# Performance work log

Measured on AMD Instinct MI355X. Metric: run time of the kernel, lower is better.

## Reference

```python
import jax, jax.numpy as jnp
import numpy as np

N, E, F, H, C = 100000, 1600000, 128, 128, 40


def setup_inputs() -> dict:
    key = jax.random.key(0)
    ks = jax.random.split(key, 9)
    feat = jax.random.normal(ks[0], (N, F), dtype=jnp.float32)
    src = jax.random.randint(ks[1], (E,), 0, N, dtype=jnp.int32)
    dst = jax.random.randint(ks[2], (E,), 0, N, dtype=jnp.int32)
    def glorot(k, fan_in, fan_out):
        s = np.float32(np.sqrt(6.0 / (fan_in + fan_out)))
        return jax.random.uniform(k, (fan_in, fan_out), jnp.float32, -s, s)
    W0 = glorot(ks[3], F, H); b0 = jnp.zeros((H,), jnp.float32)
    W1 = glorot(ks[4], H, H); b1 = jnp.zeros((H,), jnp.float32)
    W2 = glorot(ks[5], H, C); b2 = jnp.zeros((C,), jnp.float32)
    return {"feat": feat, "src": src, "dst": dst,
            "W0": W0, "b0": b0, "W1": W1, "b1": b1, "W2": W2, "b2": b2}


def _graph_conv(h, src, dst, norm_out, norm_in, W, b):
    # DGL GraphConv, norm='both': out = D_in^{-1/2} A D_out^{-1/2} h W + b
    h = h * norm_out[:, None]          # scale by source out-degree
    h = h @ W                          # transform first (in_dim >= out_dim path)
    agg = jax.ops.segment_sum(h[src], dst, num_segments=N)  # scatter-add over edges
    return agg * norm_in[:, None] + b


def reference(feat, src, dst, W0, b0, W1, b1, W2, b2):
    ones_e = jnp.ones((E,), jnp.float32)
    deg_out = jax.ops.segment_sum(ones_e, src, num_segments=N)
    deg_in = jax.ops.segment_sum(ones_e, dst, num_segments=N)
    norm_out = jnp.where(deg_out > 0, jax.lax.rsqrt(jnp.maximum(deg_out, 1.0)), 0.0)
    norm_in = jnp.where(deg_in > 0, jax.lax.rsqrt(jnp.maximum(deg_in, 1.0)), 0.0)
    h = _graph_conv(feat, src, dst, norm_out, norm_in, W0, b0)
    h = jax.nn.relu(h)
    h = _graph_conv(h, src, dst, norm_out, norm_in, W1, b1)
    h = jax.nn.relu(h)
    h = _graph_conv(h, src, dst, norm_out, norm_in, W2, b2)
    return h
```

## Files before the change

kernel.cpp:

```cpp
#include <hip/hip_runtime.h>


#define KDIM 128
#define EPB 4096

__device__ __forceinline__ float bf2f(unsigned short u) {
    unsigned int x = ((unsigned int)u) << 16;
    return __builtin_bit_cast(float, x);
}
__device__ __forceinline__ unsigned short f2bf(float f) {
    unsigned int x = __builtin_bit_cast(unsigned int, f);
    unsigned int r = x + 0x7FFFu + ((x >> 16) & 1u);
    return (unsigned short)(r >> 16);
}

__global__ __launch_bounds__(256) void b0_count(const int* __restrict__ src,
                                                const int* __restrict__ dst,
                                                int* __restrict__ gcntA,
                                                int* __restrict__ gcntB, int E, int nb) {
    __shared__ int hA[512], hB[512];
    const int t = threadIdx.x;
    for (int b = t; b < nb; b += 256) { hA[b] = 0; hB[b] = 0; }
    __syncthreads();
    const int base = blockIdx.x * EPB;
#pragma unroll
    for (int i = 0; i < 16; ++i) {
        int e = base + i * 256 + t;
        if (e < E) {
            atomicAdd(&hA[dst[e] >> 8], 1);
            atomicAdd(&hB[src[e] >> 8], 1);
        }
    }
    __syncthreads();
    for (int b = t; b < nb; b += 256) {
        if (hA[b]) atomicAdd(&gcntA[b], hA[b]);
        if (hB[b]) atomicAdd(&gcntB[b], hB[b]);
    }
}

__global__ __launch_bounds__(512) void b0b_offsets(const int* __restrict__ gcntA,
                                                   const int* __restrict__ gcntB,
                                                   int* __restrict__ offA,
                                                   int* __restrict__ offB,
                                                   int* __restrict__ gcurA,
                                                   int* __restrict__ gcurB,
                                                   int* __restrict__ row_off,
                                                   int nb, int N, int E) {
    __shared__ int sm[512];
    const int t = threadIdx.x;
    int v = (t < nb) ? gcntA[t] : 0;
    sm[t] = v;
    __syncthreads();
    for (int o = 1; o < 512; o <<= 1) {
        int x = (t >= o) ? sm[t - o] : 0;
        __syncthreads();
        sm[t] += x;
        __syncthreads();
    }
    if (t < nb) { offA[t + 1] = sm[t]; gcurA[t] = sm[t] - v; }
    if (t == 0) { offA[0] = 0; row_off[N] = E; }
    __syncthreads();
    int vb = (t < nb) ? gcntB[t] : 0;
    sm[t] = vb;
    __syncthreads();
    for (int o = 1; o < 512; o <<= 1) {
        int x = (t >= o) ? sm[t - o] : 0;
        __syncthreads();
        sm[t] += x;
        __syncthreads();
    }
    if (t < nb) { offB[t + 1] = sm[t]; gcurB[t] = sm[t] - vb; }
    if (t == 0) offB[0] = 0;
}

__global__ __launch_bounds__(256) void b1_bin(const int* __restrict__ src,
                                              const int* __restrict__ dst,
                                              int* __restrict__ gcurA,
                                              int* __restrict__ gcurB,
                                              int* __restrict__ binA,
                                              int* __restrict__ binB, int E, int nb) {
    __shared__ int hA[512], hB[512];
    const int t = threadIdx.x;
    for (int b = t; b < nb; b += 256) { hA[b] = 0; hB[b] = 0; }
    __syncthreads();
    const int base = blockIdx.x * EPB;
    int se[16], de[16];
#pragma unroll
    for (int i = 0; i < 16; ++i) {
        int e = base + i * 256 + t;
        se[i] = -1; de[i] = 0;
        if (e < E) {
            se[i] = src[e]; de[i] = dst[e];
            atomicAdd(&hA[de[i] >> 8], 1);
            atomicAdd(&hB[se[i] >> 8], 1);
        }
    }
    __syncthreads();
    for (int b = t; b < nb; b += 256) {
        int c = hA[b];
        hA[b] = c ? atomicAdd(&gcurA[b], c) : 0;
        c = hB[b];
        hB[b] = c ? atomicAdd(&gcurB[b], c) : 0;
    }
    __syncthreads();
#pragma unroll
    for (int i = 0; i < 16; ++i) {
        if (se[i] >= 0) {
            int pA = atomicAdd(&hA[de[i] >> 8], 1);
            binA[pA] = se[i] | ((de[i] & 255) << 17);
            int pB = atomicAdd(&hB[se[i] >> 8], 1);
            binB[pB] = se[i] & 255;
        }
    }
}

__global__ __launch_bounds__(256) void b2_final(const int* __restrict__ binA,
                                                const int* __restrict__ binB,
                                                const int* __restrict__ offA,
                                                const int* __restrict__ offB,
                                                int* __restrict__ ssrc,
                                                int* __restrict__ row_off,
                                                float* __restrict__ norm_in,
                                                int* __restrict__ degO, int N) {
    __shared__ int h[256], cur[256];
    const int b = blockIdx.x, t = threadIdx.x;
    const int nA0 = offA[b], cntA = offA[b + 1] - nA0;
    const int nodes = min(256, N - b * 256);

    h[t] = 0;
    __syncthreads();
    for (int k = t; k < cntA; k += 256) atomicAdd(&h[binA[nA0 + k] >> 17], 1);
    __syncthreads();

    int v = h[t];
    cur[t] = v;
    __syncthreads();
    for (int o = 1; o < 256; o <<= 1) {
        int x = (t >= o) ? cur[t - o] : 0;
        __syncthreads();
        cur[t] += x;
        __syncthreads();
    }
    const int rbase = nA0 + (cur[t] - v);
    if (t < nodes) {
        row_off[b * 256 + t] = rbase;
        norm_in[b * 256 + t] = (v > 0) ? rsqrtf((float)v) : 0.0f;
    }
    __syncthreads();
    cur[t] = rbase;
    __syncthreads();

    for (int k = t; k < cntA; k += 256) {
        int val = binA[nA0 + k];
        int pos = atomicAdd(&cur[val >> 17], 1);
        ssrc[pos] = val & 0x1FFFF;
    }

    __syncthreads();
    h[t] = 0;
    __syncthreads();
    const int nB0 = offB[b], cntB = offB[b + 1] - nB0;
    for (int k = t; k < cntB; k += 256) atomicAdd(&h[binB[nB0 + k]], 1);
    __syncthreads();
    if (t < nodes) degO[b * 256 + t] = h[t];
}

template <int M, int RPB, int CPT, bool BF16OUT>
__global__ __launch_bounds__(256) void gemm_scaled(const float* __restrict__ X,
                                                   const int* __restrict__ degO,
                                                   const float* __restrict__ W,
                                                   void* __restrict__ Tout, int nrows) {
    constexpr int CG = M / CPT;
    static_assert(CG * (RPB / 2) == 256, "thread mapping");
    __shared__ float xs[KDIM][RPB + 1];
    __shared__ float ws[64][M];

    const int t = threadIdx.x;
    const int rowbase = blockIdx.x * RPB;

    {
        constexpr int NV = RPB * (KDIM / 4) / 256;
        const float4* X4 = reinterpret_cast<const float4*>(X);
#pragma unroll
        for (int i = 0; i < NV; ++i) {
            int idx = t + i * 256;
            int rl = idx >> 5;
            int kq = idx & 31;
            int row = rowbase + rl;
            float4 v = make_float4(0.f, 0.f, 0.f, 0.f);
            float s = 0.f;
            if (row < nrows) {
                v = X4[(size_t)row * 32 + kq];
                int dv = degO[row];
                s = (dv > 0) ? rsqrtf((float)dv) : 0.0f;
            }
            xs[4 * kq + 0][rl] = v.x * s;
            xs[4 * kq + 1][rl] = v.y * s;
            xs[4 * kq + 2][rl] = v.z * s;
            xs[4 * kq + 3][rl] = v.w * s;
        }
    }

    const int rg = t / CG, cg = t % CG;
    const int r0 = 2 * rg, cb = cg * CPT;
    float acc0[CPT] = {0.f}, acc1[CPT] = {0.f};

    for (int kc = 0; kc < 2; ++kc) {
        __syncthreads();
        {
            constexpr int TOT4 = 64 * M / 4;
            const float4* W4 = reinterpret_cast<const float4*>(W);
            for (int i = t; i < TOT4; i += 256) {
                int kk = i / (M / 4), m4 = i % (M / 4);
                float4 v = W4[(size_t)(kc * 64 + kk) * (M / 4) + m4];
                ws[kk][4 * m4 + 0] = v.x;
                ws[kk][4 * m4 + 1] = v.y;
                ws[kk][4 * m4 + 2] = v.z;
                ws[kk][4 * m4 + 3] = v.w;
            }
        }
        __syncthreads();
#pragma unroll 8
        for (int k = 0; k < 64; ++k) {
            float xv0 = xs[kc * 64 + k][r0];
            float xv1 = xs[kc * 64 + k][r0 + 1];
#pragma unroll
            for (int j = 0; j < CPT; ++j) {
                float wv = ws[k][cb + j];
                acc0[j] = fmaf(xv0, wv, acc0[j]);
                acc1[j] = fmaf(xv1, wv, acc1[j]);
            }
        }
    }

    int row0 = rowbase + r0;
    if constexpr (BF16OUT) {
        static_assert(CPT == 8, "bf16 path packs 8");
        unsigned short* Tb = (unsigned short*)Tout;
        if (row0 < nrows) {
            uint4 pk;
            pk.x = f2bf(acc0[0]) | ((unsigned)f2bf(acc0[1]) << 16);
            pk.y = f2bf(acc0[2]) | ((unsigned)f2bf(acc0[3]) << 16);
            pk.z = f2bf(acc0[4]) | ((unsigned)f2bf(acc0[5]) << 16);
            pk.w = f2bf(acc0[6]) | ((unsigned)f2bf(acc0[7]) << 16);
            *reinterpret_cast<uint4*>(&Tb[(size_t)row0 * M + cb]) = pk;
        }
        if (row0 + 1 < nrows) {
            uint4 pk;
            pk.x = f2bf(acc1[0]) | ((unsigned)f2bf(acc1[1]) << 16);
            pk.y = f2bf(acc1[2]) | ((unsigned)f2bf(acc1[3]) << 16);
            pk.z = f2bf(acc1[4]) | ((unsigned)f2bf(acc1[5]) << 16);
            pk.w = f2bf(acc1[6]) | ((unsigned)f2bf(acc1[7]) << 16);
            *reinterpret_cast<uint4*>(&Tb[(size_t)(row0 + 1) * M + cb]) = pk;
        }
    } else {
        float* T = (float*)Tout;
        if (row0 < nrows) {
#pragma unroll
            for (int j = 0; j < CPT; ++j) T[(size_t)row0 * M + cb + j] = acc0[j];
        }
        if (row0 + 1 < nrows) {
#pragma unroll
            for (int j = 0; j < CPT; ++j) T[(size_t)(row0 + 1) * M + cb + j] = acc1[j];
        }
    }
}

__global__ __launch_bounds__(256) void agg_bf16(const unsigned short* __restrict__ Tb,
                                                const int* __restrict__ row_off,
                                                const int* __restrict__ ssrc,
                                                const float* __restrict__ norm_in,
                                                const float* __restrict__ bias,
                                                float* __restrict__ out, int n) {
    const int wid = (int)((blockIdx.x * blockDim.x + threadIdx.x) >> 6);
    const int lane = threadIdx.x & 63;
    if (wid >= n) return;
    const uint* T2 = reinterpret_cast<const uint*>(Tb);
    const int e0 = row_off[wid], e1 = row_off[wid + 1];
    float ax = 0.f, ay = 0.f;
    int e = e0;
    for (; e + 4 <= e1; e += 4) {
        int s0 = ssrc[e], s1 = ssrc[e + 1], s2 = ssrc[e + 2], s3 = ssrc[e + 3];
        uint v0 = T2[(size_t)s0 * 64 + lane];
        uint v1 = T2[(size_t)s1 * 64 + lane];
        uint v2 = T2[(size_t)s2 * 64 + lane];
        uint v3 = T2[(size_t)s3 * 64 + lane];
        ax += bf2f((unsigned short)v0) + bf2f((unsigned short)v1)
            + bf2f((unsigned short)v2) + bf2f((unsigned short)v3);
        ay += bf2f((unsigned short)(v0 >> 16)) + bf2f((unsigned short)(v1 >> 16))
            + bf2f((unsigned short)(v2 >> 16)) + bf2f((unsigned short)(v3 >> 16));
    }
    for (; e < e1; ++e) {
        uint v = T2[(size_t)ssrc[e] * 64 + lane];
        ax += bf2f((unsigned short)v);
        ay += bf2f((unsigned short)(v >> 16));
    }
    float ni = norm_in[wid];
    float2 b = reinterpret_cast<const float2*>(bias)[lane];
    float ox = fmaxf(ax * ni + b.x, 0.f);
    float oy = fmaxf(ay * ni + b.y, 0.f);
    reinterpret_cast<float2*>(out)[(size_t)wid * 64 + lane] = make_float2(ox, oy);
}

template <int M, bool RELU>
__global__ __launch_bounds__(256) void agg_kernel(const float* __restrict__ T,
                                                  const int* __restrict__ row_off,
                                                  const int* __restrict__ ssrc,
                                                  const float* __restrict__ norm_in,
                                                  const float* __restrict__ bias,
                                                  float* __restrict__ out, int n) {
    const int wid = (int)((blockIdx.x * blockDim.x + threadIdx.x) >> 6);
    const int lane = threadIdx.x & 63;
    if (wid >= n) return;
    constexpr int L = M / 2;
    const float2* T2 = reinterpret_cast<const float2*>(T);
    const int e0 = row_off[wid], e1 = row_off[wid + 1];
    if (lane < L) {
        float ax = 0.f, ay = 0.f;
        int e = e0;
        for (; e + 4 <= e1; e += 4) {
            int s0 = ssrc[e], s1 = ssrc[e + 1], s2 = ssrc[e + 2], s3 = ssrc[e + 3];
            float2 v0 = T2[s0 * L + lane];
            float2 v1 = T2[s1 * L + lane];
            float2 v2 = T2[s2 * L + lane];
            float2 v3 = T2[s3 * L + lane];
            ax += (v0.x + v1.x) + (v2.x + v3.x);
            ay += (v0.y + v1.y) + (v2.y + v3.y);
        }
        for (; e < e1; ++e) {
            int s = ssrc[e];
            float2 v = T2[s * L + lane];
            ax += v.x;
            ay += v.y;
        }
        float ni = norm_in[wid];
        float2 b = reinterpret_cast<const float2*>(bias)[lane];
        float ox = ax * ni + b.x;
        float oy = ay * ni + b.y;
        if (RELU) { ox = fmaxf(ox, 0.f); oy = fmaxf(oy, 0.f); }
        reinterpret_cast<float2*>(out)[(size_t)wid * L + lane] = make_float2(ox, oy);
    }
}

extern "C" void kernel_launch(void* const* d_in, const int* in_sizes, int n_in,
                              void* d_out, int out_size, void* d_ws, size_t ws_size,
                              hipStream_t stream) {
    const float* feat = (const float*)d_in[0];
    const int* src = (const int*)d_in[1];
    const int* dst = (const int*)d_in[2];
    const float* W0 = (const float*)d_in[3];
    const float* b0 = (const float*)d_in[4];
    const float* W1 = (const float*)d_in[5];
    const float* b1 = (const float*)d_in[6];
    const float* W2 = (const float*)d_in[7];
    const float* b2 = (const float*)d_in[8];
    float* outp = (float*)d_out;

    const int N = in_sizes[0] / KDIM;
    const int E = in_sizes[1];
    const int nb = (N + 255) >> 8;
    const int nblkE = (E + EPB - 1) / EPB;

    auto align = [](size_t x) { return (x + 255) & ~(size_t)255; };
    char* p = (char*)d_ws;
    int* degO      = (int*)p;    p += align((size_t)N * 4);
    float* norm_in = (float*)p;  p += align((size_t)N * 4);
    int* row_off   = (int*)p;    p += align((size_t)(N + 1) * 4);
    int* gcntA     = (int*)p;    p += 512 * 4;
    int* gcntB     = (int*)p;    p += 512 * 4;
    int* offA      = (int*)p;    p += align(513 * 4);
    int* offB      = (int*)p;    p += align(513 * 4);
    int* gcurA     = (int*)p;    p += align(512 * 4);
    int* gcurB     = (int*)p;    p += align(512 * 4);
    int* ssrc      = (int*)p;    p += align((size_t)E * 4);
    float* T       = (float*)p;  p += align((size_t)N * KDIM * 4);
    float* H       = (float*)p;  p += align((size_t)N * KDIM * 4);
    unsigned short* Tb = (unsigned short*)T;
    int* binA      = (int*)T;
    int* binB      = binA + E;
    (void)n_in; (void)out_size; (void)ws_size;

    const int aggBlocks = (int)(((size_t)N * 64 + 255) / 256);

    hipMemsetAsync(gcntA, 0, 1024 * 4, stream);

    b0_count<<<nblkE, 256, 0, stream>>>(src, dst, gcntA, gcntB, E, nb);
    b0b_offsets<<<1, 512, 0, stream>>>(gcntA, gcntB, offA, offB, gcurA, gcurB, row_off, nb, N, E);
    b1_bin<<<nblkE, 256, 0, stream>>>(src, dst, gcurA, gcurB, binA, binB, E, nb);
    b2_final<<<nb, 256, 0, stream>>>(binA, binB, offA, offB, ssrc, row_off, norm_in, degO, N);

    gemm_scaled<128, 32, 8, true><<<(N + 31) / 32, 256, 0, stream>>>(feat, degO, W0, Tb, N);
    agg_bf16<<<aggBlocks, 256, 0, stream>>>(Tb, row_off, ssrc, norm_in, b0, H, N);

    gemm_scaled<128, 32, 8, true><<<(N + 31) / 32, 256, 0, stream>>>(H, degO, W1, Tb, N);
    agg_bf16<<<aggBlocks, 256, 0, stream>>>(Tb, row_off, ssrc, norm_in, b1, H, N);

    gemm_scaled<40, 64, 5, false><<<(N + 63) / 64, 256, 0, stream>>>(H, degO, W2, T, N);
    agg_kernel<40, false><<<aggBlocks, 256, 0, stream>>>(T, row_off, ssrc, norm_in, b2, outp, N);
}
```

Measured before the change: 591.2 us.

## Use bf16 MFMA for the two 128x128 GraphConv transforms

```diff
diff --git a/kernel.cpp b/kernel.cpp
--- a/kernel.cpp
+++ b/kernel.cpp
@@ -3,6 +3,9 @@
 
 #define KDIM 128
 #define EPB 4096
+
+typedef __attribute__((ext_vector_type(4))) float f32x4;
+typedef __attribute__((ext_vector_type(8))) short short8;
 
 __device__ __forceinline__ float bf2f(unsigned short u) {
     unsigned int x = ((unsigned int)u) << 16;
@@ -165,103 +168,71 @@
     if (t < nodes) degO[b * 256 + t] = h[t];
 }
 
-template <int M, int RPB, int CPT, bool BF16OUT>
-__global__ __launch_bounds__(256) void gemm_scaled(const float* __restrict__ X,
-                                                   const int* __restrict__ degO,
-                                                   const float* __restrict__ W,
-                                                   void* __restrict__ Tout, int nrows) {
-    constexpr int CG = M / CPT;
-    static_assert(CG * (RPB / 2) == 256, "thread mapping");
-    __shared__ float xs[KDIM][RPB + 1];
-    __shared__ float ws[64][M];
-
+__global__ __launch_bounds__(256) void prep_w(const float* __restrict__ W,
+                                              unsigned int* __restrict__ Wtg) {
+    int idx = blockIdx.x * 256 + threadIdx.x;
+    if (idx < 8192) {
+        int c = idx >> 6, kk = idx & 63;
+        unsigned short lo = f2bf(W[(2 * kk) * 128 + c]);
+        unsigned short hi = f2bf(W[(2 * kk + 1) * 128 + c]);
+        Wtg[idx] = (unsigned)lo | ((unsigned)hi << 16);
+    }
+}
+
+__global__ __launch_bounds__(256, 4) void gemm_mfma(const float* __restrict__ X,
+                                                    const int* __restrict__ degO,
+                                                    const unsigned int* __restrict__ Wtg,
+                                                    unsigned short* __restrict__ Tb,
+                                                    int ntiles, int gridWaves) {
+    __shared__ unsigned int Wt[128 * 68];
     const int t = threadIdx.x;
-    const int rowbase = blockIdx.x * RPB;
-
-    {
-        constexpr int NV = RPB * (KDIM / 4) / 256;
-        const float4* X4 = reinterpret_cast<const float4*>(X);
-#pragma unroll
-        for (int i = 0; i < NV; ++i) {
-            int idx = t + i * 256;
-            int rl = idx >> 5;
-            int kq = idx & 31;
-            int row = rowbase + rl;
-            float4 v = make_float4(0.f, 0.f, 0.f, 0.f);
-            float s = 0.f;
-            if (row < nrows) {
-                v = X4[(size_t)row * 32 + kq];
-                int dv = degO[row];
-                s = (dv > 0) ? rsqrtf((float)dv) : 0.0f;
+    for (int idx = t; idx < 128 * 64; idx += 256) {
+        int c = idx >> 6, kk = idx & 63;
+        Wt[c * 68 + kk] = Wtg[idx];
+    }
+    __syncthreads();
+
+    const int lane = t & 63;
+    const int w = t >> 6;
+    const int l15 = lane & 15;
+    const int lh = lane >> 4;
+    const unsigned short* Wts = reinterpret_cast<const unsigned short*>(Wt);
+    const float4* X4 = reinterpret_cast<const float4*>(X);
+
+    for (int tile = blockIdx.x * 4 + w; tile < ntiles; tile += gridWaves) {
+        const int row = tile * 16 + l15;
+        const int dv = degO[row];
+        const float s = (dv > 0) ? rsqrtf((float)dv) : 0.0f;
+        const float4* Xr = X4 + ((size_t)row * 32 + lh * 2);
+
+        f32x4 acc[8];
+#pragma unroll
+        for (int ct = 0; ct < 8; ++ct) acc[ct] = f32x4{0.f, 0.f, 0.f, 0.f};
+
+#pragma unroll
+        for (int kc = 0; kc < 4; ++kc) {
+            float4 a0 = Xr[kc * 8];
+            float4 a1 = Xr[kc * 8 + 1];
+            short8 af;
+            af[0] = (short)f2bf(a0.x * s); af[1] = (short)f2bf(a0.y * s);
+            af[2] = (short)f2bf(a0.z * s); af[3] = (short)f2bf(a0.w * s);
+            af[4] = (short)f2bf(a1.x * s); af[5] = (short)f2bf(a1.y * s);
+            af[6] = (short)f2bf(a1.z * s); af[7] = (short)f2bf(a1.w * s);
+            const int k0 = kc * 32 + lh * 8;
+#pragma unroll
+            for (int ct = 0; ct < 8; ++ct) {
+                short8 bf = *reinterpret_cast<const short8*>(&Wts[(ct * 16 + l15) * 136 + k0]);
+                acc[ct] = __builtin_amdgcn_mfma_f32_16x16x32_bf16(af, bf, acc[ct], 0, 0, 0);
             }
-            xs[4 * kq + 0][rl] = v.x * s;
-            xs[4 * kq + 1][rl] = v.y * s;
-            xs[4 * kq + 2][rl] = v.z * s;
-            xs[4 * kq + 3][rl] = v.w * s;
-        }
-    }
-
-    const int rg = t / CG, cg = t % CG;
-    const int r0 = 2 * rg, cb = cg * CPT;
-    float acc0[CPT] = {0.f}, acc1[CPT] = {0.f};
-
-    for (int kc = 0; kc < 2; ++kc) {
-        __syncthreads();
-        {
-            constexpr int TOT4 = 64 * M / 4;
-            const float4* W4 = reinterpret_cast<const float4*>(W);
-            for (int i = t; i < TOT4; i += 256) {
-                int kk = i / (M / 4), m4 = i % (M / 4);
-                float4 v = W4[(size_t)(kc * 64 + kk) * (M / 4) + m4];
-                ws[kk][4 * m4 + 0] = v.x;
-                ws[kk][4 * m4 + 1] = v.y;
-                ws[kk][4 * m4 + 2] = v.z;
-                ws[kk][4 * m4 + 3] = v.w;
-            }
-        }
-        __syncthreads();
-#pragma unroll 8
-        for (int k = 0; k < 64; ++k) {
-            float xv0 = xs[kc * 64 + k][r0];
-            float xv1 = xs[kc * 64 + k][r0 + 1];
-#pragma unroll
-            for (int j = 0; j < CPT; ++j) {
-                float wv = ws[k][cb + j];
-                acc0[j] = fmaf(xv0, wv, acc0[j]);
-                acc1[j] = fmaf(xv1, wv, acc1[j]);
-            }
-        }
-    }
-
-    int row0 = rowbase + r0;
-    if constexpr (BF16OUT) {
-        static_assert(CPT == 8, "bf16 path packs 8");
-        unsigned short* Tb = (unsigned short*)Tout;
-        if (row0 < nrows) {
-            uint4 pk;
-            pk.x = f2bf(acc0[0]) | ((unsigned)f2bf(acc0[1]) << 16);
-            pk.y = f2bf(acc0[2]) | ((unsigned)f2bf(acc0[3]) << 16);
-            pk.z = f2bf(acc0[4]) | ((unsigned)f2bf(acc0[5]) << 16);
-            pk.w = f2bf(acc0[6]) | ((unsigned)f2bf(acc0[7]) << 16);
-            *reinterpret_cast<uint4*>(&Tb[(size_t)row0 * M + cb]) = pk;
-        }
-        if (row0 + 1 < nrows) {
-            uint4 pk;
-            pk.x = f2bf(acc1[0]) | ((unsigned)f2bf(acc1[1]) << 16);
-            pk.y = f2bf(acc1[2]) | ((unsigned)f2bf(acc1[3]) << 16);
-            pk.z = f2bf(acc1[4]) | ((unsigned)f2bf(acc1[5]) << 16);
-            pk.w = f2bf(acc1[6]) | ((unsigned)f2bf(acc1[7]) << 16);
-            *reinterpret_cast<uint4*>(&Tb[(size_t)(row0 + 1) * M + cb]) = pk;
-        }
-    } else {
-        float* T = (float*)Tout;
-        if (row0 < nrows) {
-#pragma unroll
-            for (int j = 0; j < CPT; ++j) T[(size_t)row0 * M + cb + j] = acc0[j];
-        }
-        if (row0 + 1 < nrows) {
-#pragma unroll
-            for (int j = 0; j < CPT; ++j) T[(size_t)(row0 + 1) * M + cb + j] = acc1[j];
+        }
+
+        const int rbase = tile * 16 + lh * 4;
+#pragma unroll
+        for (int ct = 0; ct < 8; ++ct) {
+            const int col = ct * 16 + l15;
+#pragma unroll
+            for (int r = 0; r < 4; ++r)
+                Tb[(size_t)(rbase + r) * 128 + col] = f2bf(acc[ct][r]);
         }
     }
 }
@@ -300,6 +271,85 @@
     float ox = fmaxf(ax * ni + b.x, 0.f);
     float oy = fmaxf(ay * ni + b.y, 0.f);
     reinterpret_cast<float2*>(out)[(size_t)wid * 64 + lane] = make_float2(ox, oy);
+}
+
+template <int M, int RPB, int CPT>
+__global__ __launch_bounds__(256) void gemm_scaled(const float* __restrict__ X,
+                                                   const int* __restrict__ degO,
+                                                   const float* __restrict__ W,
+                                                   float* __restrict__ T, int nrows) {
+    constexpr int CG = M / CPT;
+    static_assert(CG * (RPB / 2) == 256, "thread mapping");
+    __shared__ float xs[KDIM][RPB + 1];
+    __shared__ float ws[64][M];
+
+    const int t = threadIdx.x;
+    const int rowbase = blockIdx.x * RPB;
+
+    {
+        constexpr int NV = RPB * (KDIM / 4) / 256;
+        const float4* X4 = reinterpret_cast<const float4*>(X);
+#pragma unroll
+        for (int i = 0; i < NV; ++i) {
+            int idx = t + i * 256;
+            int rl = idx >> 5;
+            int kq = idx & 31;
+            int row = rowbase + rl;
+            float4 v = make_float4(0.f, 0.f, 0.f, 0.f);
+            float s = 0.f;
+            if (row < nrows) {
+                v = X4[(size_t)row * 32 + kq];
+                int dv = degO[row];
+                s = (dv > 0) ? rsqrtf((float)dv) : 0.0f;
+            }
+            xs[4 * kq + 0][rl] = v.x * s;
+            xs[4 * kq + 1][rl] = v.y * s;
+            xs[4 * kq + 2][rl] = v.z * s;
+            xs[4 * kq + 3][rl] = v.w * s;
+        }
+    }
+
+    const int rg = t / CG, cg = t % CG;
+    const int r0 = 2 * rg, cb = cg * CPT;
+    float acc0[CPT] = {0.f}, acc1[CPT] = {0.f};
+
+    for (int kc = 0; kc < 2; ++kc) {
+        __syncthreads();
+        {
+            constexpr int TOT4 = 64 * M / 4;
+            const float4* W4 = reinterpret_cast<const float4*>(W);
+            for (int i = t; i < TOT4; i += 256) {
+                int kk = i / (M / 4), m4 = i % (M / 4);
+                float4 v = W4[(size_t)(kc * 64 + kk) * (M / 4) + m4];
+                ws[kk][4 * m4 + 0] = v.x;
+                ws[kk][4 * m4 + 1] = v.y;
+                ws[kk][4 * m4 + 2] = v.z;
+                ws[kk][4 * m4 + 3] = v.w;
+            }
+        }
+        __syncthreads();
+#pragma unroll 8
+        for (int k = 0; k < 64; ++k) {
+            float xv0 = xs[kc * 64 + k][r0];
+            float xv1 = xs[kc * 64 + k][r0 + 1];
+#pragma unroll
+            for (int j = 0; j < CPT; ++j) {
+                float wv = ws[k][cb + j];
+                acc0[j] = fmaf(xv0, wv, acc0[j]);
+                acc1[j] = fmaf(xv1, wv, acc1[j]);
+            }
+        }
+    }
+
+    int row0 = rowbase + r0;
+    if (row0 < nrows) {
+#pragma unroll
+        for (int j = 0; j < CPT; ++j) T[(size_t)row0 * M + cb + j] = acc0[j];
+    }
+    if (row0 + 1 < nrows) {
+#pragma unroll
+        for (int j = 0; j < CPT; ++j) T[(size_t)(row0 + 1) * M + cb + j] = acc1[j];
+    }
 }
 
 template <int M, bool RELU>
@@ -372,6 +422,8 @@
     int* offB      = (int*)p;    p += align(513 * 4);
     int* gcurA     = (int*)p;    p += align(512 * 4);
     int* gcurB     = (int*)p;    p += align(512 * 4);
+    unsigned int* W0t = (unsigned int*)p;  p += align(8192 * 4);
+    unsigned int* W1t = (unsigned int*)p;  p += align(8192 * 4);
     int* ssrc      = (int*)p;    p += align((size_t)E * 4);
     float* T       = (float*)p;  p += align((size_t)N * KDIM * 4);
     float* H       = (float*)p;  p += align((size_t)N * KDIM * 4);
@@ -381,20 +433,26 @@
     (void)n_in; (void)out_size; (void)ws_size;
 
     const int aggBlocks = (int)(((size_t)N * 64 + 255) / 256);
+    const int ntiles = N / 16;
+    const int gBlocks = (ntiles + 3) / 4;
+    const int gridWaves = gBlocks * 4;
 
     hipMemsetAsync(gcntA, 0, 1024 * 4, stream);
+
+    prep_w<<<32, 256, 0, stream>>>(W0, W0t);
+    prep_w<<<32, 256, 0, stream>>>(W1, W1t);
 
     b0_count<<<nblkE, 256, 0, stream>>>(src, dst, gcntA, gcntB, E, nb);
     b0b_offsets<<<1, 512, 0, stream>>>(gcntA, gcntB, offA, offB, gcurA, gcurB, row_off, nb, N, E);
     b1_bin<<<nblkE, 256, 0, stream>>>(src, dst, gcurA, gcurB, binA, binB, E, nb);
     b2_final<<<nb, 256, 0, stream>>>(binA, binB, offA, offB, ssrc, row_off, norm_in, degO, N);
 
-    gemm_scaled<128, 32, 8, true><<<(N + 31) / 32, 256, 0, stream>>>(feat, degO, W0, Tb, N);
+    gemm_mfma<<<gBlocks, 256, 0, stream>>>(feat, degO, W0t, Tb, ntiles, gridWaves);
     agg_bf16<<<aggBlocks, 256, 0, stream>>>(Tb, row_off, ssrc, norm_in, b0, H, N);
 
-    gemm_scaled<128, 32, 8, true><<<(N + 31) / 32, 256, 0, stream>>>(H, degO, W1, Tb, N);
+    gemm_mfma<<<gBlocks, 256, 0, stream>>>(H, degO, W1t, Tb, ntiles, gridWaves);
     agg_bf16<<<aggBlocks, 256, 0, stream>>>(Tb, row_off, ssrc, norm_in, b1, H, N);
 
-    gemm_scaled<40, 64, 5, false><<<(N + 63) / 64, 256, 0, stream>>>(H, degO, W2, T, N);
+    gemm_scaled<40, 64, 5><<<(N + 63) / 64, 256, 0, stream>>>(H, degO, W2, T, N);
     agg_kernel<40, false><<<aggBlocks, 256, 0, stream>>>(T, row_off, ssrc, norm_in, b2, outp, N);
 }
```

Measured after the change: 535.1 us. 1.1x faster.
